# Optimization experiments

Hardware: AMD Instinct MI355X
Metric: run time of the kernel (lower is better)

Reference implementation:

```python
import jax, jax.numpy as jnp
import numpy as np

N_HEAD = 16
HEAD_DIM = 64
EMBED_DIM = N_HEAD * HEAD_DIM  # 1024


def setup_inputs() -> dict:
    key = jax.random.key(0)
    k1, k2, k3, k4, k5 = jax.random.split(key, 5)
    B, L, D = 4, 2048, 1024
    x = jax.random.normal(k1, (B, L, D), dtype=jnp.float32)
    # EnsembleLinear(input_dim, head_dim, n_head*3): per-ensemble weight/bias
    Wqkv = jax.random.normal(k2, (3 * N_HEAD, D, HEAD_DIM), dtype=jnp.float32) * 0.02
    bqkv = jax.random.normal(k3, (3 * N_HEAD, HEAD_DIM), dtype=jnp.float32) * 0.02
    Wp = jax.random.normal(k4, (EMBED_DIM, EMBED_DIM), dtype=jnp.float32) * 0.02
    bp = jax.random.normal(k5, (EMBED_DIM,), dtype=jnp.float32) * 0.02
    return {"x": x, "Wqkv": Wqkv, "bqkv": bqkv, "Wp": Wp, "bp": bp}


def reference(x, Wqkv, bqkv, Wp, bp):
    B, L, _ = x.shape
    # EnsembleLinear: (3*n_head, B, L, head_dim)
    ctx = jnp.einsum('bld,edh->eblh', x, Wqkv) + bqkv[:, None, None, :]
    q, k, v = jnp.split(ctx, 3, axis=0)  # each (n_head, B, L, head_dim)
    # NOTE: original code does `o /= head_dim ** (-0.5)` i.e. multiplies by sqrt(head_dim);
    # reproduced faithfully.
    scale = jnp.asarray(HEAD_DIM ** 0.5, dtype=x.dtype)
    scores = jnp.einsum('hbqd,hbkd->hbqk', q, k) * scale  # (n_head, B, L, L)
    attn = jax.nn.softmax(scores, axis=-1)
    av = jnp.einsum('hbqk,hbkd->hbqd', attn, v)  # (n_head, B, L, head_dim)
    av = av.transpose(1, 2, 0, 3).reshape(B, L, EMBED_DIM)  # (B, L, embed_dim)
    out = av @ Wp.T + bp  # proj Linear
    return out
```

## Files before the change

kernel.cpp:

```cpp
#include <hip/hip_runtime.h>
#include <stdint.h>

typedef _Float16 f16;
typedef _Float16 f16x8 __attribute__((ext_vector_type(8)));
typedef _Float16 f16x4 __attribute__((ext_vector_type(4)));
typedef float floatx4 __attribute__((ext_vector_type(4)));
typedef uint32_t u32x2 __attribute__((ext_vector_type(2)));

static __device__ __forceinline__ floatx4 mfma32(f16x8 a, f16x8 b, floatx4 c) {
  return __builtin_amdgcn_mfma_f32_16x16x32_f16(a, b, c, 0, 0, 0);
}
static __device__ __forceinline__ floatx4 mfma16(f16x4 a, f16x4 b, floatx4 c) {
  return __builtin_amdgcn_mfma_f32_16x16x16f16(a, b, c, 0, 0, 0);
}
static __device__ __forceinline__ uint32_t pack2(f16 lo, f16 hi) {
  return (uint32_t)__builtin_bit_cast(uint16_t, lo) |
         ((uint32_t)__builtin_bit_cast(uint16_t, hi) << 16);
}

static __device__ __forceinline__ f16x8 load8(const void* p, size_t e, int raw) {
  if (!raw) return *(const f16x8*)((const f16*)p + e);
  const float* f = (const float*)p + e;
  floatx4 a = *(const floatx4*)f, b = *(const floatx4*)(f + 4);
  f16x8 r;
  r[0] = (f16)a[0]; r[1] = (f16)a[1]; r[2] = (f16)a[2]; r[3] = (f16)a[3];
  r[4] = (f16)b[0]; r[5] = (f16)b[1]; r[6] = (f16)b[2]; r[7] = (f16)b[3];
  return r;
}
static __device__ __forceinline__ float load1(const void* p, size_t e, int raw) {
  return raw ? ((const float*)p)[e] : (float)((const f16*)p)[e];
}

__global__ __launch_bounds__(256) void transpose_group(const float* __restrict__ W,
                                                       const float* __restrict__ bq,
                                                       f16* __restrict__ Wt,
                                                       f16* __restrict__ biasc,
                                                       int g0, int G) {
  __shared__ f16 T[64 * 80];
  const int s = blockIdx.x;
  const int d0 = blockIdx.y * 64;
  const int tid = threadIdx.x;
  if (s >= 3 * G) {
#pragma unroll
    for (int st = 0; st < 2; ++st) {
      int j = tid + st * 256;
      int hh = j >> 3, dc = j & 7;
      f16x8 z = {};
      *(f16x8*)&Wt[(size_t)(s * 64 + hh) * 1024 + d0 + dc * 8] = z;
    }
    if (blockIdx.y == 0 && tid < 64) biasc[s * 64 + tid] = (f16)0.f;
    return;
  }
  const int e = (s / G) * 16 + g0 + (s % G);
#pragma unroll
  for (int st = 0; st < 2; ++st) {
    int j = tid + st * 256;
    int dl = j >> 3, hc = j & 7;
    f16x8 v = load8(W, ((size_t)e * 1024 + d0 + dl) * 64 + hc * 8, 1);
#pragma unroll
    for (int jj = 0; jj < 8; ++jj) T[(hc * 8 + jj) * 80 + dl] = v[jj];
  }
  __syncthreads();
#pragma unroll
  for (int st = 0; st < 2; ++st) {
    int j = tid + st * 256;
    int hh = j >> 3, dc = j & 7;
    f16x8 o = *(const f16x8*)&T[hh * 80 + dc * 8];
    *(f16x8*)&Wt[(size_t)(s * 64 + hh) * 1024 + d0 + dc * 8] = o;
  }
  if (blockIdx.y == 0 && tid < 64)
    biasc[s * 64 + tid] = (f16)bq[(size_t)e * 64 + tid];
}

__global__ __launch_bounds__(256) void gemm_bt(const void* __restrict__ A, size_t a0,
                                               int aRaw, const void* __restrict__ B,
                                               int bRaw, const void* __restrict__ bias,
                                               int biasRaw, void* __restrict__ C,
                                               size_t c0, int cHalf,
                                               int M, int N, int K, int ldc) {
  __shared__ f16 As[128 * 72];
  __shared__ f16 Bs[128 * 72];
  const int tid = threadIdx.x;
  const int wave = tid >> 6, lane = tid & 63;
  const int c = lane & 15, g = lane >> 4;
  const int bm = blockIdx.y * 128, bn = blockIdx.x * 128;
  const int wm = (wave >> 1) * 64, wn = (wave & 1) * 64;

  floatx4 acc[4][4] = {};

  for (int k0 = 0; k0 < K; k0 += 64) {
#pragma unroll
    for (int s = 0; s < 4; ++s) {
      int j = tid + s * 256;
      int row = j >> 3, ch = j & 7;
      f16x8 va = load8(A, a0 + (size_t)(bm + row) * K + k0 + ch * 8, aRaw);
      f16x8 vb = load8(B, (size_t)(bn + row) * K + k0 + ch * 8, bRaw);
      *(f16x8*)&As[row * 72 + ch * 8] = va;
      *(f16x8*)&Bs[row * 72 + ch * 8] = vb;
    }
    __syncthreads();
#pragma unroll
    for (int kk = 0; kk < 2; ++kk) {
      f16x8 af[4], bfr[4];
#pragma unroll
      for (int i = 0; i < 4; ++i) {
        af[i]  = *(const f16x8*)&As[(wm + i * 16 + c) * 72 + (kk * 4 + g) * 8];
        bfr[i] = *(const f16x8*)&Bs[(wn + i * 16 + c) * 72 + (kk * 4 + g) * 8];
      }
#pragma unroll
      for (int i = 0; i < 4; ++i)
#pragma unroll
        for (int jn = 0; jn < 4; ++jn)
          acc[i][jn] = mfma32(af[i], bfr[jn], acc[i][jn]);
    }
    __syncthreads();
  }

  float bv[4];
#pragma unroll
  for (int jn = 0; jn < 4; ++jn)
    bv[jn] = load1(bias, (size_t)(bn + wn + jn * 16 + c), biasRaw);
#pragma unroll
  for (int i = 0; i < 4; ++i) {
#pragma unroll
    for (int r = 0; r < 4; ++r) {
      size_t row = (size_t)(bm + wm + i * 16 + g * 4 + r);
#pragma unroll
      for (int jn = 0; jn < 4; ++jn) {
        float v = acc[i][jn][r] + bv[jn];
        size_t idx = c0 + row * ldc + (bn + wn + jn * 16 + c);
        if (cHalf) ((f16*)C)[idx] = (f16)v; else ((float*)C)[idx] = v;
      }
    }
  }
}

__global__ __launch_bounds__(256) void attn_kernel(const f16* __restrict__ qkv,
                                                   f16* __restrict__ av,
                                                   int ld, int kbase, int vbase,
                                                   int gh0, int b0) {
  const int hh = blockIdx.y;
  const int z = blockIdx.z;
  const int q0 = blockIdx.x * 128;
  const f16* base = qkv + (size_t)z * 2048 * ld;
  const f16* Qp = base + hh * 64;
  const f16* Kp = base + kbase + hh * 64;
  const f16* Vp = base + vbase + hh * 64;

  __shared__ __align__(16) char smem[18432];
  f16* Ks = (f16*)smem;
  uint32_t* Vs = (uint32_t*)(smem + 9216);

  const int tid = threadIdx.x;
  const int wave = tid >> 6, lane = tid & 63;
  const int c = lane & 15, g = lane >> 4;

  f16x8 qf[2][2];
#pragma unroll
  for (int st = 0; st < 2; ++st) {
    const f16* qrow = Qp + (size_t)(q0 + wave * 32 + st * 16 + c) * ld;
    qf[st][0] = *(const f16x8*)(qrow + g * 8);
    qf[st][1] = *(const f16x8*)(qrow + 32 + g * 8);
  }

  float m_i[2] = {-1e30f, -1e30f}, l_i[2] = {0.f, 0.f};
  floatx4 acc_o[2][4] = {};

  const int vp = tid & 31, vch = tid >> 5;

  for (int t = 0; t < 32; ++t) {
    const int kv0 = t * 64;
#pragma unroll
    for (int it = 0; it < 2; ++it) {
      int j = tid + it * 256;
      int row = j >> 3, ch = j & 7;
      *(f16x8*)&Ks[row * 72 + ch * 8] =
          *(const f16x8*)(Kp + (size_t)(kv0 + row) * ld + ch * 8);
    }
    {
      const f16* ra = Vp + (size_t)(kv0 + 2 * vp) * ld + vch * 8;
      f16x8 a = *(const f16x8*)ra;
      f16x8 bvv = *(const f16x8*)(ra + ld);
#pragma unroll
      for (int jj = 0; jj < 8; ++jj)
        Vs[(vch * 8 + jj) * 34 + vp] = pack2(a[jj], bvv[jj]);
    }
    __syncthreads();

    f16x8 kf[4][2];
#pragma unroll
    for (int nb = 0; nb < 4; ++nb)
#pragma unroll
      for (int kk = 0; kk < 2; ++kk)
        kf[nb][kk] = *(const f16x8*)&Ks[(nb * 16 + c) * 72 + (kk * 4 + g) * 8];

    f16x4 pfrag[2][4];
#pragma unroll
    for (int st = 0; st < 2; ++st) {
      floatx4 sacc[4] = {};
#pragma unroll
      for (int kk = 0; kk < 2; ++kk)
#pragma unroll
        for (int nb = 0; nb < 4; ++nb)
          sacc[nb] = mfma32(kf[nb][kk], qf[st][kk], sacc[nb]);

      float sv[4][4];
      float mx = -1e30f;
#pragma unroll
      for (int nb = 0; nb < 4; ++nb)
#pragma unroll
        for (int r = 0; r < 4; ++r) {
          sv[nb][r] = sacc[nb][r] * 8.0f;
          mx = fmaxf(mx, sv[nb][r]);
        }
      mx = fmaxf(mx, __shfl_xor(mx, 16, 64));
      mx = fmaxf(mx, __shfl_xor(mx, 32, 64));
      float mnew = fmaxf(m_i[st], mx);
      float alpha = __expf(m_i[st] - mnew);
      float rs = 0.f;
#pragma unroll
      for (int nb = 0; nb < 4; ++nb)
#pragma unroll
        for (int r = 0; r < 4; ++r) {
          sv[nb][r] = __expf(sv[nb][r] - mnew);
          rs += sv[nb][r];
        }
      rs += __shfl_xor(rs, 16, 64);
      rs += __shfl_xor(rs, 32, 64);
      m_i[st] = mnew;
      l_i[st] = l_i[st] * alpha + rs;
#pragma unroll
      for (int db = 0; db < 4; ++db) acc_o[st][db] *= alpha;
#pragma unroll
      for (int nb = 0; nb < 4; ++nb) {
        f16x4 pf = {(f16)sv[nb][0], (f16)sv[nb][1], (f16)sv[nb][2], (f16)sv[nb][3]};
        pfrag[st][nb] = pf;
      }
    }

#pragma unroll
    for (int nb = 0; nb < 4; ++nb)
#pragma unroll
      for (int db = 0; db < 4; ++db) {
        u32x2 raw = *(const u32x2*)&Vs[(db * 16 + c) * 34 + nb * 8 + 2 * g];
        f16x4 vf = __builtin_bit_cast(f16x4, raw);
#pragma unroll
        for (int st = 0; st < 2; ++st)
          acc_o[st][db] = mfma16(vf, pfrag[st][nb], acc_o[st][db]);
      }
    __syncthreads();
  }

  f16* Ot = (f16*)smem;
  float inv[2] = {1.0f / l_i[0], 1.0f / l_i[1]};
#pragma unroll
  for (int st = 0; st < 2; ++st)
#pragma unroll
    for (int db = 0; db < 4; ++db)
#pragma unroll
      for (int r = 0; r < 4; ++r)
        Ot[(wave * 32 + st * 16 + c) * 72 + db * 16 + g * 4 + r] =
            (f16)(acc_o[st][db][r] * inv[st]);
  __syncthreads();
#pragma unroll
  for (int it = 0; it < 4; ++it) {
    int j = tid + it * 256;
    int row = j >> 3, ch = j & 7;
    *(f16x8*)&av[(size_t)((b0 + z) * 2048 + q0 + row) * 1024 + (gh0 + hh) * 64 + ch * 8] =
        *(const f16x8*)&Ot[row * 72 + ch * 8];
  }
}

__global__ __launch_bounds__(256) void copyk(const f16* __restrict__ src,
                                             f16* __restrict__ dst, long n8) {
  long i = (long)blockIdx.x * 256 + threadIdx.x;
  if (i < n8) ((f16x8*)dst)[i] = ((const f16x8*)src)[i];
}

extern "C" void kernel_launch(void* const* d_in, const int* in_sizes, int n_in,
                              void* d_out, int out_size, void* d_ws, size_t ws_size,
                              hipStream_t stream) {
  (void)in_sizes; (void)n_in; (void)out_size;
  const float* x    = (const float*)d_in[0];
  const float* Wqkv = (const float*)d_in[1];
  const float* bqkv = (const float*)d_in[2];
  const float* Wp   = (const float*)d_in[3];
  const float* bp   = (const float*)d_in[4];
  float* out = (float*)d_out;
  char* ws = (char*)d_ws;
  const size_t avail = ws_size;

  if (avail >= (size_t)67108864) {
    f16* Wqkvt = (f16*)d_out;
    f16* biasc = (f16*)d_out + (size_t)3072 * 1024;
    f16* qkv = (f16*)ws;
    f16* av  = (f16*)(ws + 50331648);
    transpose_group<<<dim3(48, 16), 256, 0, stream>>>(Wqkv, bqkv, Wqkvt, biasc, 0, 16);
    gemm_bt<<<dim3(24, 64), 256, 0, stream>>>(x, 0, 1, Wqkvt, 0, biasc, 0, qkv, 0, 1,
                                              8192, 3072, 1024, 3072);
    attn_kernel<<<dim3(16, 16, 4), 256, 0, stream>>>(qkv, av, 3072, 1024, 2048, 0, 0);
    gemm_bt<<<dim3(8, 64), 256, 0, stream>>>(av, 0, 0, Wp, 1, bp, 1, out, 0, 0,
                                             8192, 1024, 1024, 1024);
    return;
  }

  auto need = [](size_t N, size_t Mr) { return N * 2 * (1024 + Mr + 1); };
  int G; bool perBatch = false;
  if      (avail >= need(3072, 8192)) G = 16;
  else if (avail >= need(1536, 8192)) G = 8;
  else if (avail >= need(768, 8192))  G = 4;
  else if (avail >= need(384, 8192))  G = 2;
  else if (avail >= need(256, 8192))  G = 1;
  else { G = 1; perBatch = true; }
  const int N = (G == 1) ? 256 : G * 192;
  const size_t Mr = perBatch ? 2048 : 8192;

  f16* Wt    = (f16*)ws;
  f16* qkvg  = (f16*)(ws + (size_t)N * 1024 * 2);
  f16* biasc = (f16*)(ws + (size_t)N * 1024 * 2 + Mr * N * 2);
  f16* av    = (f16*)d_out;
  const int tgrid = 3 * G + (G == 1 ? 1 : 0);

  for (int g0 = 0; g0 < 16; g0 += G) {
    transpose_group<<<dim3(tgrid, 16), 256, 0, stream>>>(Wqkv, bqkv, Wt, biasc, g0, G);
    if (!perBatch) {
      gemm_bt<<<dim3(N / 128, 64), 256, 0, stream>>>(x, 0, 1, Wt, 0, biasc, 0, qkvg, 0, 1,
                                                     8192, N, 1024, N);
      attn_kernel<<<dim3(16, G, 4), 256, 0, stream>>>(qkvg, av, N, G * 64, 2 * G * 64, g0, 0);
    } else {
      for (int b = 0; b < 4; ++b) {
        gemm_bt<<<dim3(N / 128, 16), 256, 0, stream>>>(x, (size_t)b * 2048 * 1024, 1, Wt,
                                                       0, biasc, 0, qkvg, 0, 1,
                                                       2048, N, 1024, N);
        attn_kernel<<<dim3(16, G, 1), 256, 0, stream>>>(qkvg, av, N, G * 64, 2 * G * 64, g0, b);
      }
    }
  }

  f16* chunkbuf = qkvg;
  const int rows = perBatch ? 512 : 1024;
  for (int r0 = 8192 - rows; r0 >= 0; r0 -= rows) {
    long n8 = (long)rows * 1024 / 8;
    copyk<<<dim3((int)(n8 / 256)), 256, 0, stream>>>(av + (size_t)r0 * 1024, chunkbuf, n8);
    gemm_bt<<<dim3(8, rows / 128), 256, 0, stream>>>(chunkbuf, 0, 0, Wp, 1, bp, 1, out,
                                                     (size_t)r0 * 1024, 0,
                                                     rows, 1024, 1024, 1024);
  }
}
```

Baseline: 413.5 us.

## Use async global-to-LDS loads with XOR swizzle and pre-convert x to fp16

Adds a separate pass that converts x to fp16 into spare output memory, so the QKV GEMM can load fp16 operands straight into LDS with global_load_lds and an XOR-swizzled layout instead of staging through registers. The projection GEMM uses the async path for its fp16 A operand only, since Wp is still fp32. The sqrt(head_dim) scale is folded into the Q weights and bias during the transpose, which removes a multiply per score in attention. The cost is an extra conversion kernel and fp16 rounding of the scaled Q weights.

```diff
diff --git a/kernel.cpp b/kernel.cpp
--- a/kernel.cpp
+++ b/kernel.cpp
@@ -7,6 +7,9 @@
 typedef float floatx4 __attribute__((ext_vector_type(4)));
 typedef uint32_t u32x2 __attribute__((ext_vector_type(2)));
 
+#define AS1 __attribute__((address_space(1)))
+#define AS3 __attribute__((address_space(3)))
+
 static __device__ __forceinline__ floatx4 mfma32(f16x8 a, f16x8 b, floatx4 c) {
   return __builtin_amdgcn_mfma_f32_16x16x32_f16(a, b, c, 0, 0, 0);
 }
@@ -16,6 +19,9 @@
 static __device__ __forceinline__ uint32_t pack2(f16 lo, f16 hi) {
   return (uint32_t)__builtin_bit_cast(uint16_t, lo) |
          ((uint32_t)__builtin_bit_cast(uint16_t, hi) << 16);
+}
+static __device__ __forceinline__ void gload_lds16(const void* g, void* l) {
+  __builtin_amdgcn_global_load_lds((AS1 void*)g, (AS3 void*)l, 16, 0, 0);
 }
 
 static __device__ __forceinline__ f16x8 load8(const void* p, size_t e, int raw) {
@@ -29,6 +35,13 @@
 }
 static __device__ __forceinline__ float load1(const void* p, size_t e, int raw) {
   return raw ? ((const float*)p)[e] : (float)((const f16*)p)[e];
+}
+
+__global__ __launch_bounds__(256) void cvt_f16(const float* __restrict__ src,
+                                               f16* __restrict__ dst, long n8) {
+  long i = (long)blockIdx.x * 256 + threadIdx.x;
+  if (i >= n8) return;
+  *(f16x8*)(dst + i * 8) = load8(src, (size_t)i * 8, 1);
 }
 
 __global__ __launch_bounds__(256) void transpose_group(const float* __restrict__ W,
@@ -52,13 +65,14 @@
     return;
   }
   const int e = (s / G) * 16 + g0 + (s % G);
+  const float scale = (s < G) ? 8.f : 1.f;
 #pragma unroll
   for (int st = 0; st < 2; ++st) {
     int j = tid + st * 256;
     int dl = j >> 3, hc = j & 7;
-    f16x8 v = load8(W, ((size_t)e * 1024 + d0 + dl) * 64 + hc * 8, 1);
-#pragma unroll
-    for (int jj = 0; jj < 8; ++jj) T[(hc * 8 + jj) * 80 + dl] = v[jj];
+    const float* f = &W[((size_t)e * 1024 + d0 + dl) * 64 + hc * 8];
+#pragma unroll
+    for (int jj = 0; jj < 8; ++jj) T[(hc * 8 + jj) * 80 + dl] = (f16)(f[jj] * scale);
   }
   __syncthreads();
 #pragma unroll
@@ -69,17 +83,20 @@
     *(f16x8*)&Wt[(size_t)(s * 64 + hh) * 1024 + d0 + dc * 8] = o;
   }
   if (blockIdx.y == 0 && tid < 64)
-    biasc[s * 64 + tid] = (f16)bq[(size_t)e * 64 + tid];
-}
-
+    biasc[s * 64 + tid] = (f16)(bq[(size_t)e * 64 + tid] * scale);
+}
+
+template <int AASYNC, int BASYNC>
 __global__ __launch_bounds__(256) void gemm_bt(const void* __restrict__ A, size_t a0,
                                                int aRaw, const void* __restrict__ B,
                                                int bRaw, const void* __restrict__ bias,
                                                int biasRaw, void* __restrict__ C,
                                                size_t c0, int cHalf,
                                                int M, int N, int K, int ldc) {
-  __shared__ f16 As[128 * 72];
-  __shared__ f16 Bs[128 * 72];
+  constexpr int AST = AASYNC ? 64 : 72;
+  constexpr int BST = BASYNC ? 64 : 72;
+  __shared__ f16 As[128 * AST];
+  __shared__ f16 Bs[128 * BST];
   const int tid = threadIdx.x;
   const int wave = tid >> 6, lane = tid & 63;
   const int c = lane & 15, g = lane >> 4;
@@ -89,14 +106,43 @@
   floatx4 acc[4][4] = {};
 
   for (int k0 = 0; k0 < K; k0 += 64) {
-#pragma unroll
-    for (int s = 0; s < 4; ++s) {
-      int j = tid + s * 256;
-      int row = j >> 3, ch = j & 7;
-      f16x8 va = load8(A, a0 + (size_t)(bm + row) * K + k0 + ch * 8, aRaw);
-      f16x8 vb = load8(B, (size_t)(bn + row) * K + k0 + ch * 8, bRaw);
-      *(f16x8*)&As[row * 72 + ch * 8] = va;
-      *(f16x8*)&Bs[row * 72 + ch * 8] = vb;
+    if (AASYNC) {
+      const f16* Af = (const f16*)A;
+#pragma unroll
+      for (int t = 0; t < 4; ++t) {
+        int j = (wave * 4 + t) * 64 + lane;
+        int row = j >> 3;
+        int kc = (j & 7) ^ (row & 7);
+        gload_lds16(Af + a0 + (size_t)(bm + row) * K + k0 + kc * 8,
+                    As + (wave * 4 + t) * 512);
+      }
+    } else {
+#pragma unroll
+      for (int s = 0; s < 4; ++s) {
+        int j = tid + s * 256;
+        int row = j >> 3, ch = j & 7;
+        *(f16x8*)&As[row * 72 + ch * 8] =
+            load8(A, a0 + (size_t)(bm + row) * K + k0 + ch * 8, aRaw);
+      }
+    }
+    if (BASYNC) {
+      const f16* Bf = (const f16*)B;
+#pragma unroll
+      for (int t = 0; t < 4; ++t) {
+        int j = (wave * 4 + t) * 64 + lane;
+        int row = j >> 3;
+        int kc = (j & 7) ^ (row & 7);
+        gload_lds16(Bf + (size_t)(bn + row) * K + k0 + kc * 8,
+                    Bs + (wave * 4 + t) * 512);
+      }
+    } else {
+#pragma unroll
+      for (int s = 0; s < 4; ++s) {
+        int j = tid + s * 256;
+        int row = j >> 3, ch = j & 7;
+        *(f16x8*)&Bs[row * 72 + ch * 8] =
+            load8(B, (size_t)(bn + row) * K + k0 + ch * 8, bRaw);
+      }
     }
     __syncthreads();
 #pragma unroll
@@ -104,8 +150,12 @@
       f16x8 af[4], bfr[4];
 #pragma unroll
       for (int i = 0; i < 4; ++i) {
-        af[i]  = *(const f16x8*)&As[(wm + i * 16 + c) * 72 + (kk * 4 + g) * 8];
-        bfr[i] = *(const f16x8*)&Bs[(wn + i * 16 + c) * 72 + (kk * 4 + g) * 8];
+        int ar = wm + i * 16 + c;
+        int apos = AASYNC ? ((kk * 4 + g) ^ (ar & 7)) : (kk * 4 + g);
+        af[i] = *(const f16x8*)&As[ar * AST + apos * 8];
+        int br = wn + i * 16 + c;
+        int bpos = BASYNC ? ((kk * 4 + g) ^ (br & 7)) : (kk * 4 + g);
+        bfr[i] = *(const f16x8*)&Bs[br * BST + bpos * 8];
       }
 #pragma unroll
       for (int i = 0; i < 4; ++i)
@@ -210,7 +260,7 @@
       for (int nb = 0; nb < 4; ++nb)
 #pragma unroll
         for (int r = 0; r < 4; ++r) {
-          sv[nb][r] = sacc[nb][r] * 8.0f;
+          sv[nb][r] = sacc[nb][r];
           mx = fmaxf(mx, sv[nb][r]);
         }
       mx = fmaxf(mx, __shfl_xor(mx, 16, 64));
@@ -292,15 +342,17 @@
 
   if (avail >= (size_t)67108864) {
     f16* Wqkvt = (f16*)d_out;
-    f16* biasc = (f16*)d_out + (size_t)3072 * 1024;
+    f16* biasc = (f16*)((char*)d_out + 6291456);
+    f16* xh    = (f16*)((char*)d_out + 6297600);
     f16* qkv = (f16*)ws;
     f16* av  = (f16*)(ws + 50331648);
+    cvt_f16<<<dim3(4096), 256, 0, stream>>>(x, xh, 1048576);
     transpose_group<<<dim3(48, 16), 256, 0, stream>>>(Wqkv, bqkv, Wqkvt, biasc, 0, 16);
-    gemm_bt<<<dim3(24, 64), 256, 0, stream>>>(x, 0, 1, Wqkvt, 0, biasc, 0, qkv, 0, 1,
-                                              8192, 3072, 1024, 3072);
+    gemm_bt<1, 1><<<dim3(24, 64), 256, 0, stream>>>(xh, 0, 0, Wqkvt, 0, biasc, 0,
+                                                    qkv, 0, 1, 8192, 3072, 1024, 3072);
     attn_kernel<<<dim3(16, 16, 4), 256, 0, stream>>>(qkv, av, 3072, 1024, 2048, 0, 0);
-    gemm_bt<<<dim3(8, 64), 256, 0, stream>>>(av, 0, 0, Wp, 1, bp, 1, out, 0, 0,
-                                             8192, 1024, 1024, 1024);
+    gemm_bt<1, 0><<<dim3(8, 64), 256, 0, stream>>>(av, 0, 0, Wp, 1, bp, 1,
+                                                   out, 0, 0, 8192, 1024, 1024, 1024);
     return;
   }
 
@@ -324,14 +376,14 @@
   for (int g0 = 0; g0 < 16; g0 += G) {
     transpose_group<<<dim3(tgrid, 16), 256, 0, stream>>>(Wqkv, bqkv, Wt, biasc, g0, G);
     if (!perBatch) {
-      gemm_bt<<<dim3(N / 128, 64), 256, 0, stream>>>(x, 0, 1, Wt, 0, biasc, 0, qkvg, 0, 1,
-                                                     8192, N, 1024, N);
+      gemm_bt<0, 0><<<dim3(N / 128, 64), 256, 0, stream>>>(x, 0, 1, Wt, 0, biasc, 0,
+                                                           qkvg, 0, 1, 8192, N, 1024, N);
       attn_kernel<<<dim3(16, G, 4), 256, 0, stream>>>(qkvg, av, N, G * 64, 2 * G * 64, g0, 0);
     } else {
       for (int b = 0; b < 4; ++b) {
-        gemm_bt<<<dim3(N / 128, 16), 256, 0, stream>>>(x, (size_t)b * 2048 * 1024, 1, Wt,
-                                                       0, biasc, 0, qkvg, 0, 1,
-                                                       2048, N, 1024, N);
+        gemm_bt<0, 0><<<dim3(N / 128, 16), 256, 0, stream>>>(x, (size_t)b * 2048 * 1024, 1,
+                                                             Wt, 0, biasc, 0, qkvg, 0, 1,
+                                                             2048, N, 1024, N);
         attn_kernel<<<dim3(16, G, 1), 256, 0, stream>>>(qkvg, av, N, G * 64, 2 * G * 64, g0, b);
       }
     }
@@ -342,8 +394,8 @@
   for (int r0 = 8192 - rows; r0 >= 0; r0 -= rows) {
     long n8 = (long)rows * 1024 / 8;
     copyk<<<dim3((int)(n8 / 256)), 256, 0, stream>>>(av + (size_t)r0 * 1024, chunkbuf, n8);
-    gemm_bt<<<dim3(8, rows / 128), 256, 0, stream>>>(chunkbuf, 0, 0, Wp, 1, bp, 1, out,
-                                                     (size_t)r0 * 1024, 0,
-                                                     rows, 1024, 1024, 1024);
-  }
-}
+    gemm_bt<0, 0><<<dim3(8, rows / 128), 256, 0, stream>>>(chunkbuf, 0, 0, Wp, 1, bp, 1,
+                                                           out, (size_t)r0 * 1024, 0,
+                                                           rows, 1024, 1024, 1024);
+  }
+}
```

Result: faster. 353.2 us (-14.6%).
